# Performance work log

Measured on AMD Instinct MI355X. Metric: run time of the kernel, lower is better.

Reference implementation:

```python
import jax, jax.numpy as jnp
import numpy as np

N, D, E, K = 65536, 2048, 64, 8
EPS = 1e-5


def setup_inputs() -> dict:
    key = jax.random.key(0)
    kx, kw = jax.random.split(key)
    x = jax.random.normal(kx, (N, D), dtype=jnp.float32)
    # nn.Linear(input_size, num_experts, bias=False) weight: [E, D]
    W = jax.random.normal(kw, (E, D), dtype=jnp.float32) * (1.0 / np.sqrt(D))
    return {"x": x, "W": W}


def _l1_normalize(v):
    # torch F.normalize(p=1, dim=0): v / max(||v||_1, 1e-12)
    return v / jnp.maximum(jnp.sum(jnp.abs(v)), 1e-12)


def reference(x, W):
    # router logits: [N, E] in float32 (matches .float() in torch code)
    logits = (x @ W.T).astype(jnp.float32)
    top_v, top_i = jax.lax.top_k(logits, K)            # [N, K]
    top_k_gates = jax.nn.softmax(top_v, axis=-1).astype(x.dtype)
    # training-branch aux loss (compute_aux_loss)
    probs = jax.nn.softmax(logits, axis=-1)            # [N, E]
    rows = jnp.arange(logits.shape[0])[:, None]
    dense_gates = jnp.zeros_like(probs, dtype=top_k_gates.dtype).at[rows, top_i].set(top_k_gates)
    probs_sum = probs.sum(0)                           # [E]
    freq = (dense_gates > 0).astype(jnp.float32).sum(0)  # [E]
    # log(sum(exp(logits)) + eps)^2 summed, computed stably
    lse = jnp.logaddexp(jax.scipy.special.logsumexp(logits, axis=-1), jnp.log(EPS))
    zloss = jnp.sum(lse ** 2) / logits.shape[0]
    switchloss = E * jnp.sum(_l1_normalize(probs_sum) * _l1_normalize(freq))
    loss = switchloss + 0.1 * zloss
    return top_i, top_k_gates, loss
```

## Files before the change

### kernel.cpp

```cpp
#include <hip/hip_runtime.h>
#include <math.h>

#define NROWS 65536
#define DDIM 2048
#define NEXP 64
#define TOPK 8

constexpr int BM = 128;
constexpr int BK = 32;
constexpr int NTH = 256;
constexpr int NSTEP = DDIM / BK;
constexpr int CAP = 8192;
constexpr float THR = 3e-4f;

typedef short bf16x8 __attribute__((ext_vector_type(8)));
typedef float f32x4 __attribute__((ext_vector_type(4)));

__device__ inline unsigned short bfround(float f) {
    union { float f; unsigned u; } v; v.f = f;
    unsigned r = (v.u + 0x7fffu + ((v.u >> 16) & 1u)) >> 16;
    return (unsigned short)r;
}
__device__ inline float bf2f(unsigned short h) {
    union { unsigned u; float f; } v; v.u = ((unsigned)h) << 16;
    return v.f;
}
__device__ inline void cvt8(const float4& A, const float4& B, bf16x8& h, bf16x8& l) {
    float f[8] = {A.x, A.y, A.z, A.w, B.x, B.y, B.z, B.w};
#pragma unroll
    for (int j = 0; j < 8; ++j) {
        unsigned short hh = bfround(f[j]);
        h[j] = (short)hh;
        l[j] = (short)bfround(f[j] - bf2f(hh));
    }
}

__global__ __launch_bounds__(NTH, 1)
void gate_kernel(const float* __restrict__ x, const float* __restrict__ W,
                 float* __restrict__ out_idx, float* __restrict__ out_gate,
                 float* __restrict__ g_psum, float* __restrict__ g_freq,
                 float* __restrict__ g_zsum, int* __restrict__ g_cnt,
                 int* __restrict__ g_rows, float* __restrict__ g_logits)
{
    __shared__ __align__(16) short Bfrag[2][2][4][64][8];
    __shared__ float psum_s[NEXP];
    __shared__ float fcnt_s[NEXP];

    const int tid = threadIdx.x;
    const int w = tid >> 6;
    const int lane = tid & 63;
    const int g = lane >> 4;
    const int c = lane & 15;
    const int row0 = blockIdx.x * BM + w * 32;

    if (tid < NEXP) { psum_s[tid] = 0.f; fcnt_s[tid] = 0.f; }

    const int se = tid >> 2;
    const int skg = tid & 3;
    const int sct = se >> 4;
    const int slane = (se & 15) + (skg << 4);

    const float* xr0 = x + (size_t)(row0 + c) * DDIM + g * 8;
    const float* xr1 = x + (size_t)(row0 + 16 + c) * DDIM + g * 8;
    const float* wp  = W + (size_t)se * DDIM + skg * 8;

    f32x4 acc[2][4];
#pragma unroll
    for (int rt = 0; rt < 2; ++rt)
#pragma unroll
        for (int ct = 0; ct < 4; ++ct) acc[rt][ct] = (f32x4){0.f, 0.f, 0.f, 0.f};

    float4 xa[2][2], xb[2][2];

    auto stageB = [&](int k0, int buf) {
        float4 a = *reinterpret_cast<const float4*>(wp + k0);
        float4 b = *reinterpret_cast<const float4*>(wp + k0 + 4);
        bf16x8 h, l;
        cvt8(a, b, h, l);
        *reinterpret_cast<bf16x8*>(&Bfrag[buf][0][sct][slane][0]) = h;
        *reinterpret_cast<bf16x8*>(&Bfrag[buf][1][sct][slane][0]) = l;
    };

    xa[0][0] = *reinterpret_cast<const float4*>(xr0);
    xa[0][1] = *reinterpret_cast<const float4*>(xr0 + 4);
    xa[1][0] = *reinterpret_cast<const float4*>(xr1);
    xa[1][1] = *reinterpret_cast<const float4*>(xr1 + 4);
    stageB(0, 0);
    __syncthreads();

    for (int t = 0; t < NSTEP; ++t) {
        const int buf = t & 1;
        const int kn = (t + 1) * BK;
        if (t + 1 < NSTEP) {
            xb[0][0] = *reinterpret_cast<const float4*>(xr0 + kn);
            xb[0][1] = *reinterpret_cast<const float4*>(xr0 + kn + 4);
            xb[1][0] = *reinterpret_cast<const float4*>(xr1 + kn);
            xb[1][1] = *reinterpret_cast<const float4*>(xr1 + kn + 4);
            stageB(kn, buf ^ 1);
        }
        bf16x8 ah[2], al[2];
        cvt8(xa[0][0], xa[0][1], ah[0], al[0]);
        cvt8(xa[1][0], xa[1][1], ah[1], al[1]);
        bf16x8 bh[4], bl[4];
#pragma unroll
        for (int ct = 0; ct < 4; ++ct) {
            bh[ct] = *reinterpret_cast<const bf16x8*>(&Bfrag[buf][0][ct][lane][0]);
            bl[ct] = *reinterpret_cast<const bf16x8*>(&Bfrag[buf][1][ct][lane][0]);
        }
#pragma unroll
        for (int rt = 0; rt < 2; ++rt)
#pragma unroll
            for (int ct = 0; ct < 4; ++ct) {
                acc[rt][ct] = __builtin_amdgcn_mfma_f32_16x16x32_bf16(
                    ah[rt], bh[ct], acc[rt][ct], 0, 0, 0);
                acc[rt][ct] = __builtin_amdgcn_mfma_f32_16x16x32_bf16(
                    ah[rt], bl[ct], acc[rt][ct], 0, 0, 0);
                acc[rt][ct] = __builtin_amdgcn_mfma_f32_16x16x32_bf16(
                    al[rt], bh[ct], acc[rt][ct], 0, 0, 0);
            }
#pragma unroll
        for (int rt = 0; rt < 2; ++rt)
#pragma unroll
            for (int i = 0; i < 2; ++i) xa[rt][i] = xb[rt][i];
        __syncthreads();
    }

    float pcol[4] = {0.f, 0.f, 0.f, 0.f};
    float zsq_acc = 0.f;

#pragma unroll
    for (int rt = 0; rt < 2; ++rt) {
#pragma unroll
        for (int reg = 0; reg < 4; ++reg) {
            const int row = row0 + rt * 16 + g * 4 + reg;
            float ld[4];
#pragma unroll
            for (int ct = 0; ct < 4; ++ct) ld[ct] = acc[rt][ct][reg];

            float tv[9]; int ti[9];
#pragma unroll
            for (int p = 0; p < 9; ++p) {
                float bv = -3.4e38f; int bgi = 127;
#pragma unroll
                for (int ct = 0; ct < 4; ++ct) {
                    int e = ct * 16 + c;
                    if (ld[ct] > bv) { bv = ld[ct]; bgi = e; }
                }
#pragma unroll
                for (int m = 1; m < 16; m <<= 1) {
                    float ov = __shfl_xor(bv, m, 16);
                    int ogi = __shfl_xor(bgi, m, 16);
                    if (ov > bv || (ov == bv && ogi < bgi)) { bv = ov; bgi = ogi; }
                }
                tv[p] = bv; ti[p] = bgi;
#pragma unroll
                for (int ct = 0; ct < 4; ++ct)
                    if (bgi == ct * 16 + c) ld[ct] = -3.4e38f;
            }

            float mg = 3.4e38f;
#pragma unroll
            for (int p = 0; p < 8; ++p) mg = fminf(mg, tv[p] - tv[p + 1]);
            if (mg < THR) {
                int idx = 0;
                if (c == 0) idx = atomicAdd(g_cnt, 1);
                idx = __shfl(idx, (lane >> 4) << 4, 64);
                if (idx < CAP) {
                    if (c == 0) g_rows[idx] = row;
#pragma unroll
                    for (int ct = 0; ct < 4; ++ct)
                        g_logits[(size_t)idx * NEXP + ct * 16 + c] = acc[rt][ct][reg];
                }
            }

            const float m0 = tv[0];
            float pe[4], ps = 0.f;
#pragma unroll
            for (int ct = 0; ct < 4; ++ct) {
                pe[ct] = expf(acc[rt][ct][reg] - m0);
                ps += pe[ct];
            }
            float s = ps;
#pragma unroll
            for (int m = 1; m < 16; m <<= 1) s += __shfl_xor(s, m, 16);
            const float inv_s = 1.f / s;
#pragma unroll
            for (int ct = 0; ct < 4; ++ct) pcol[ct] += pe[ct] * inv_s;

            if (c == 0) {
                float lsef = m0 + logf(s);
                const float lb = -11.512925464970229f;
                float mx = fmaxf(lsef, lb), mn = fminf(lsef, lb);
                float z = mx + log1pf(expf(mn - mx));
                zsq_acc += z * z;
            }

            float gs = 0.f;
#pragma unroll
            for (int p = 0; p < 8; ++p) gs += expf(tv[p] - m0);
            if (c < 8) {
                float mytv = tv[0]; int myti = ti[0];
#pragma unroll
                for (int p = 1; p < 8; ++p)
                    if (c == p) { mytv = tv[p]; myti = ti[p]; }
                const size_t base = (size_t)row * TOPK;
                out_idx[base + c] = (float)myti;
                out_gate[base + c] = expf(mytv - m0) / gs;
                atomicAdd(&fcnt_s[myti], 1.f);
            }
        }
    }

#pragma unroll
    for (int off = 32; off > 0; off >>= 1) zsq_acc += __shfl_down(zsq_acc, off, 64);
    if (lane == 0) atomicAdd(g_zsum, zsq_acc);

#pragma unroll
    for (int ct = 0; ct < 4; ++ct) atomicAdd(&psum_s[ct * 16 + c], pcol[ct]);
    __syncthreads();
    if (tid < NEXP) {
        atomicAdd(&g_psum[tid], psum_s[tid]);
        atomicAdd(&g_freq[tid], fcnt_s[tid]);
    }
}

__global__ __launch_bounds__(256, 1)
void fixup_kernel(const float* __restrict__ x, const float* __restrict__ W,
                  float* __restrict__ out_idx, float* __restrict__ out_gate,
                  const int* __restrict__ g_cnt, const int* __restrict__ g_rows,
                  const float* __restrict__ g_logits)
{
    const int n = min(*g_cnt, CAP);
    const int tid = threadIdx.x;
    const int grp = tid >> 5;
    const int gl = tid & 31;
    __shared__ float sLog[NEXP];
    __shared__ double sD[16];
    __shared__ int sCand[16];
    __shared__ int sNc;

    for (int i = blockIdx.x; i < n; i += gridDim.x) {
        const int row = g_rows[i];
        if (tid < NEXP) sLog[tid] = g_logits[(size_t)i * NEXP + tid];
        if (tid == 0) sNc = 0;
        __syncthreads();

        if (tid < NEXP) {
            const int lane = tid;
            const float myv = sLog[lane];
            float vv = myv;
            float v9 = 0.f;
#pragma unroll
            for (int p = 0; p < 9; ++p) {
                float bv = vv; int bgi = lane;
#pragma unroll
                for (int m = 1; m < 64; m <<= 1) {
                    float ov = __shfl_xor(bv, m, 64);
                    int ogi = __shfl_xor(bgi, m, 64);
                    if (ov > bv || (ov == bv && ogi < bgi)) { bv = ov; bgi = ogi; }
                }
                if (lane == bgi) vv = -3.4e38f;
                v9 = bv;
            }
            if (myv >= v9 - THR) {
                int slot = atomicAdd(&sNc, 1);
                if (slot < 16) sCand[slot] = lane;
            }
        }
        __syncthreads();
        const int nc = min(sNc, 16);

        const float* xr = x + (size_t)row * DDIM;
        for (int cb = 0; cb < nc; cb += 8) {
            const int ci = cb + grp;
            if (ci < nc) {
                const float* wr = W + (size_t)sCand[ci] * DDIM;
                double p0 = 0.0, p1 = 0.0, p2 = 0.0, p3 = 0.0;
#pragma unroll
                for (int j = 0; j < 16; ++j) {
                    const int k = j * 128 + gl * 4;
                    float4 wv = *reinterpret_cast<const float4*>(wr + k);
                    float4 xv = *reinterpret_cast<const float4*>(xr + k);
                    p0 = fma((double)xv.x, (double)wv.x, p0);
                    p1 = fma((double)xv.y, (double)wv.y, p1);
                    p2 = fma((double)xv.z, (double)wv.z, p2);
                    p3 = fma((double)xv.w, (double)wv.w, p3);
                }
                double s = (p0 + p1) + (p2 + p3);
#pragma unroll
                for (int m = 1; m < 32; m <<= 1) s += __shfl_xor(s, m, 32);
                if (gl == 0) sD[ci] = s;
            }
        }
        __syncthreads();

        if (tid < NEXP) {
            const int lane = tid;
            double v = (lane < nc) ? sD[lane] : -HUGE_VAL;
            int id = (lane < nc) ? sCand[lane] : 1000;
            double tv[8]; int ti[8];
#pragma unroll
            for (int p = 0; p < 8; ++p) {
                double bv = v; int bgi = id;
#pragma unroll
                for (int m = 1; m < 64; m <<= 1) {
                    double ov = __shfl_xor(bv, m, 64);
                    int ogi = __shfl_xor(bgi, m, 64);
                    if (ov > bv || (ov == bv && ogi < bgi)) { bv = ov; bgi = ogi; }
                }
                tv[p] = bv; ti[p] = bgi;
                if (id == bgi) v = -HUGE_VAL;
            }

            const double m0 = tv[0];
            double gs = 0.0, ge[8];
#pragma unroll
            for (int j = 0; j < 8; ++j) { ge[j] = exp(tv[j] - m0); gs += ge[j]; }
            if (lane < 8) {
                double myge = ge[0]; int myti = ti[0];
#pragma unroll
                for (int j = 1; j < 8; ++j)
                    if (lane == j) { myge = ge[j]; myti = ti[j]; }
                const size_t base = (size_t)row * TOPK;
                out_idx[base + lane] = (float)myti;
                out_gate[base + lane] = (float)(myge / gs);
            }
        }
        __syncthreads();
    }
}

__global__ void finalize_kernel(const float* __restrict__ g_psum,
                                const float* __restrict__ g_freq,
                                const float* __restrict__ g_zsum,
                                float* __restrict__ out_loss)
{
    const int lane = threadIdx.x & 63;
    float p = g_psum[lane], f = g_freq[lane];
    float sp = p, sf = f;
#pragma unroll
    for (int m = 1; m < 64; m <<= 1) { sp += __shfl_xor(sp, m, 64); sf += __shfl_xor(sf, m, 64); }
    sp = fmaxf(sp, 1e-12f);
    sf = fmaxf(sf, 1e-12f);
    float term = (p / sp) * (f / sf);
#pragma unroll
    for (int m = 1; m < 64; m <<= 1) term += __shfl_xor(term, m, 64);
    if (lane == 0)
        out_loss[0] = (float)NEXP * term + 0.1f * (g_zsum[0] / (float)NROWS);
}

extern "C" void kernel_launch(void* const* d_in, const int* in_sizes, int n_in,
                              void* d_out, int out_size, void* d_ws, size_t ws_size,
                              hipStream_t stream)
{
    const float* x = (const float*)d_in[0];
    const float* W = (const float*)d_in[1];
    float* out = (float*)d_out;
    float* out_idx  = out;
    float* out_gate = out + (size_t)NROWS * TOPK;
    float* out_loss = out + (size_t)2 * NROWS * TOPK;

    float* acc    = (float*)d_ws;
    int*   cnt    = (int*)d_ws + 129;
    int*   rows   = (int*)d_ws + 130;
    float* logits = (float*)d_ws + 130 + CAP;
    hipMemsetAsync(d_ws, 0, 130 * sizeof(float), stream);

    gate_kernel<<<NROWS / BM, NTH, 0, stream>>>(
        x, W, out_idx, out_gate, acc, acc + NEXP, acc + 2 * NEXP, cnt, rows, logits);
    fixup_kernel<<<2048, 256, 0, stream>>>(x, W, out_idx, out_gate, cnt, rows, logits);
    finalize_kernel<<<1, 64, 0, stream>>>(acc, acc + NEXP, acc + 2 * NEXP, out_loss);
}
```

Measured before the change: 237.5 us.

## Precompute bf16 split W fragments and fix ambiguous rows in-block

A new prep kernel converts W once into hi/lo bf16 MFMA fragments in workspace. The main GEMM loop then reads them straight from global/L2 instead of converting and staging W through shared memory every step, which also removes the per-step barrier. Rows with near-tied top-k logits are now recomputed in fp64 inside the gate kernel using per-wave shared buffers, with only overflow rows going to a smaller fixup launch. The trade-offs are an extra kernel launch, more global fragment loads per wave, and serial fp64 work in the gate kernel's tail.

```diff
diff --git a/kernel.cpp b/kernel.cpp
--- a/kernel.cpp
+++ b/kernel.cpp
@@ -7,11 +7,12 @@
 #define TOPK 8
 
 constexpr int BM = 128;
-constexpr int BK = 32;
 constexpr int NTH = 256;
-constexpr int NSTEP = DDIM / BK;
-constexpr int CAP = 8192;
+constexpr int NSTEP = 64;
+constexpr int CAP = 1024;
+constexpr int FCAP = 16;
 constexpr float THR = 3e-4f;
+constexpr int WFRAG_STEP = 4096;
 
 typedef short bf16x8 __attribute__((ext_vector_type(8)));
 typedef float f32x4 __attribute__((ext_vector_type(4)));
@@ -35,16 +36,37 @@
     }
 }
 
+__global__ __launch_bounds__(256)
+void prep_kernel(const float* __restrict__ W, short* __restrict__ wfrag)
+{
+    const int t = blockIdx.x;
+    const int tid = threadIdx.x;
+    const int ct = tid >> 6, lane = tid & 63;
+    const int e = ct * 16 + (lane & 15);
+    const int k = t * 32 + (lane >> 4) * 8;
+    const float* wp = W + (size_t)e * DDIM + k;
+    float4 a = *reinterpret_cast<const float4*>(wp);
+    float4 b = *reinterpret_cast<const float4*>(wp + 4);
+    bf16x8 h, l;
+    cvt8(a, b, h, l);
+    short* base = wfrag + (size_t)t * WFRAG_STEP;
+    *reinterpret_cast<bf16x8*>(base + (ct * 64 + lane) * 8) = h;
+    *reinterpret_cast<bf16x8*>(base + 2048 + (ct * 64 + lane) * 8) = l;
+}
+
 __global__ __launch_bounds__(NTH, 1)
-void gate_kernel(const float* __restrict__ x, const float* __restrict__ W,
+void gate_kernel(const float* __restrict__ x, const short* __restrict__ wfrag,
+                 const float* __restrict__ W,
                  float* __restrict__ out_idx, float* __restrict__ out_gate,
                  float* __restrict__ g_psum, float* __restrict__ g_freq,
                  float* __restrict__ g_zsum, int* __restrict__ g_cnt,
                  int* __restrict__ g_rows, float* __restrict__ g_logits)
 {
-    __shared__ __align__(16) short Bfrag[2][2][4][64][8];
     __shared__ float psum_s[NEXP];
     __shared__ float fcnt_s[NEXP];
+    __shared__ float fRow[4][FCAP][NEXP];
+    __shared__ int fId[4][FCAP];
+    __shared__ int fN[4];
 
     const int tid = threadIdx.x;
     const int w = tid >> 6;
@@ -54,15 +76,11 @@
     const int row0 = blockIdx.x * BM + w * 32;
 
     if (tid < NEXP) { psum_s[tid] = 0.f; fcnt_s[tid] = 0.f; }
-
-    const int se = tid >> 2;
-    const int skg = tid & 3;
-    const int sct = se >> 4;
-    const int slane = (se & 15) + (skg << 4);
+    if (lane == 0) fN[w] = 0;
+    __syncthreads();
 
     const float* xr0 = x + (size_t)(row0 + c) * DDIM + g * 8;
     const float* xr1 = x + (size_t)(row0 + 16 + c) * DDIM + g * 8;
-    const float* wp  = W + (size_t)se * DDIM + skg * 8;
 
     f32x4 acc[2][4];
 #pragma unroll
@@ -71,42 +89,29 @@
         for (int ct = 0; ct < 4; ++ct) acc[rt][ct] = (f32x4){0.f, 0.f, 0.f, 0.f};
 
     float4 xa[2][2], xb[2][2];
-
-    auto stageB = [&](int k0, int buf) {
-        float4 a = *reinterpret_cast<const float4*>(wp + k0);
-        float4 b = *reinterpret_cast<const float4*>(wp + k0 + 4);
-        bf16x8 h, l;
-        cvt8(a, b, h, l);
-        *reinterpret_cast<bf16x8*>(&Bfrag[buf][0][sct][slane][0]) = h;
-        *reinterpret_cast<bf16x8*>(&Bfrag[buf][1][sct][slane][0]) = l;
-    };
-
     xa[0][0] = *reinterpret_cast<const float4*>(xr0);
     xa[0][1] = *reinterpret_cast<const float4*>(xr0 + 4);
     xa[1][0] = *reinterpret_cast<const float4*>(xr1);
     xa[1][1] = *reinterpret_cast<const float4*>(xr1 + 4);
-    stageB(0, 0);
-    __syncthreads();
 
     for (int t = 0; t < NSTEP; ++t) {
-        const int buf = t & 1;
-        const int kn = (t + 1) * BK;
+        const short* wt = wfrag + (size_t)t * WFRAG_STEP;
+        bf16x8 bh[4], bl[4];
+#pragma unroll
+        for (int ct = 0; ct < 4; ++ct) {
+            bh[ct] = *reinterpret_cast<const bf16x8*>(wt + (ct * 64 + lane) * 8);
+            bl[ct] = *reinterpret_cast<const bf16x8*>(wt + 2048 + (ct * 64 + lane) * 8);
+        }
+        const int kn = (t + 1) * 32;
         if (t + 1 < NSTEP) {
             xb[0][0] = *reinterpret_cast<const float4*>(xr0 + kn);
             xb[0][1] = *reinterpret_cast<const float4*>(xr0 + kn + 4);
             xb[1][0] = *reinterpret_cast<const float4*>(xr1 + kn);
             xb[1][1] = *reinterpret_cast<const float4*>(xr1 + kn + 4);
-            stageB(kn, buf ^ 1);
         }
         bf16x8 ah[2], al[2];
         cvt8(xa[0][0], xa[0][1], ah[0], al[0]);
         cvt8(xa[1][0], xa[1][1], ah[1], al[1]);
-        bf16x8 bh[4], bl[4];
-#pragma unroll
-        for (int ct = 0; ct < 4; ++ct) {
-            bh[ct] = *reinterpret_cast<const bf16x8*>(&Bfrag[buf][0][ct][lane][0]);
-            bl[ct] = *reinterpret_cast<const bf16x8*>(&Bfrag[buf][1][ct][lane][0]);
-        }
 #pragma unroll
         for (int rt = 0; rt < 2; ++rt)
 #pragma unroll
@@ -122,7 +127,6 @@
         for (int rt = 0; rt < 2; ++rt)
 #pragma unroll
             for (int i = 0; i < 2; ++i) xa[rt][i] = xb[rt][i];
-        __syncthreads();
     }
 
     float pcol[4] = {0.f, 0.f, 0.f, 0.f};
@@ -161,15 +165,26 @@
             float mg = 3.4e38f;
 #pragma unroll
             for (int p = 0; p < 8; ++p) mg = fminf(mg, tv[p] - tv[p + 1]);
-            if (mg < THR) {
-                int idx = 0;
-                if (c == 0) idx = atomicAdd(g_cnt, 1);
-                idx = __shfl(idx, (lane >> 4) << 4, 64);
-                if (idx < CAP) {
-                    if (c == 0) g_rows[idx] = row;
+            const bool flagged = (mg < THR);
+            if (flagged) {
+                int slot = 0;
+                if (c == 0) slot = atomicAdd(&fN[w], 1);
+                slot = __shfl(slot, (lane >> 4) << 4, 64);
+                if (slot < FCAP) {
+                    if (c == 0) fId[w][slot] = row;
 #pragma unroll
                     for (int ct = 0; ct < 4; ++ct)
-                        g_logits[(size_t)idx * NEXP + ct * 16 + c] = acc[rt][ct][reg];
+                        fRow[w][slot][ct * 16 + c] = acc[rt][ct][reg];
+                } else {
+                    int idx = 0;
+                    if (c == 0) idx = atomicAdd(g_cnt, 1);
+                    idx = __shfl(idx, (lane >> 4) << 4, 64);
+                    if (idx < CAP) {
+                        if (c == 0) g_rows[idx] = row;
+#pragma unroll
+                        for (int ct = 0; ct < 4; ++ct)
+                            g_logits[(size_t)idx * NEXP + ct * 16 + c] = acc[rt][ct][reg];
+                    }
                 }
             }
 
@@ -206,8 +221,85 @@
                 const size_t base = (size_t)row * TOPK;
                 out_idx[base + c] = (float)myti;
                 out_gate[base + c] = expf(mytv - m0) / gs;
-                atomicAdd(&fcnt_s[myti], 1.f);
-            }
+                if (!flagged) atomicAdd(&fcnt_s[myti], 1.f);
+            }
+        }
+    }
+
+    const int nf = min(fN[w], FCAP);
+    for (int s = 0; s < nf; ++s) {
+        const int R = fId[w][s];
+        const float myLog = fRow[w][s][lane];
+        float vv = myLog, v9 = 0.f;
+#pragma unroll
+        for (int p = 0; p < 9; ++p) {
+            float bv = vv; int bgi = lane;
+#pragma unroll
+            for (int m = 1; m < 64; m <<= 1) {
+                float ov = __shfl_xor(bv, m, 64);
+                int ogi = __shfl_xor(bgi, m, 64);
+                if (ov > bv || (ov == bv && ogi < bgi)) { bv = ov; bgi = ogi; }
+            }
+            v9 = bv;
+            if (lane == bgi) vv = -3.4e38f;
+        }
+        const bool cand = (myLog >= v9 - THR);
+        unsigned long long cm = __ballot(cand);
+
+        const float* xrw = x + (size_t)R * DDIM;
+        float4 xv[8];
+#pragma unroll
+        for (int j = 0; j < 8; ++j)
+            xv[j] = *reinterpret_cast<const float4*>(xrw + j * 256 + lane * 4);
+
+        double myD = -HUGE_VAL;
+        unsigned long long m2 = cm;
+        while (m2) {
+            const int e = (int)__ffsll((unsigned long long)m2) - 1;
+            m2 &= (m2 - 1);
+            const float* wrp = W + (size_t)e * DDIM;
+            double p0 = 0.0, p1 = 0.0, p2 = 0.0, p3 = 0.0;
+#pragma unroll
+            for (int j = 0; j < 8; ++j) {
+                float4 wv = *reinterpret_cast<const float4*>(wrp + j * 256 + lane * 4);
+                p0 = fma((double)xv[j].x, (double)wv.x, p0);
+                p1 = fma((double)xv[j].y, (double)wv.y, p1);
+                p2 = fma((double)xv[j].z, (double)wv.z, p2);
+                p3 = fma((double)xv[j].w, (double)wv.w, p3);
+            }
+            double sd = (p0 + p1) + (p2 + p3);
+#pragma unroll
+            for (int m = 1; m < 64; m <<= 1) sd += __shfl_xor(sd, m, 64);
+            if (lane == e) myD = sd;
+        }
+
+        double v = cand ? myD : -HUGE_VAL;
+        double tvd[8]; int tid8[8];
+#pragma unroll
+        for (int p = 0; p < 8; ++p) {
+            double bv = v; int bgi = lane;
+#pragma unroll
+            for (int m = 1; m < 64; m <<= 1) {
+                double ov = __shfl_xor(bv, m, 64);
+                int ogi = __shfl_xor(bgi, m, 64);
+                if (ov > bv || (ov == bv && ogi < bgi)) { bv = ov; bgi = ogi; }
+            }
+            tvd[p] = bv; tid8[p] = bgi;
+            if (lane == bgi) v = -HUGE_VAL;
+        }
+        const double m0 = tvd[0];
+        double gsum = 0.0, ge[8];
+#pragma unroll
+        for (int j = 0; j < 8; ++j) { ge[j] = exp(tvd[j] - m0); gsum += ge[j]; }
+        if (lane < 8) {
+            double myge = ge[0]; int myti = tid8[0];
+#pragma unroll
+            for (int j = 1; j < 8; ++j)
+                if (lane == j) { myge = ge[j]; myti = tid8[j]; }
+            const size_t base = (size_t)R * TOPK;
+            out_idx[base + lane] = (float)myti;
+            out_gate[base + lane] = (float)(myge / gsum);
+            atomicAdd(&fcnt_s[myti], 1.f);
         }
     }
 
@@ -227,6 +319,7 @@
 __global__ __launch_bounds__(256, 1)
 void fixup_kernel(const float* __restrict__ x, const float* __restrict__ W,
                   float* __restrict__ out_idx, float* __restrict__ out_gate,
+                  float* __restrict__ g_freq,
                   const int* __restrict__ g_cnt, const int* __restrict__ g_rows,
                   const float* __restrict__ g_logits)
 {
@@ -248,8 +341,7 @@
         if (tid < NEXP) {
             const int lane = tid;
             const float myv = sLog[lane];
-            float vv = myv;
-            float v9 = 0.f;
+            float vv = myv, v9 = 0.f;
 #pragma unroll
             for (int p = 0; p < 9; ++p) {
                 float bv = vv; int bgi = lane;
@@ -280,16 +372,16 @@
                 for (int j = 0; j < 16; ++j) {
                     const int k = j * 128 + gl * 4;
                     float4 wv = *reinterpret_cast<const float4*>(wr + k);
-                    float4 xv = *reinterpret_cast<const float4*>(xr + k);
-                    p0 = fma((double)xv.x, (double)wv.x, p0);
-                    p1 = fma((double)xv.y, (double)wv.y, p1);
-                    p2 = fma((double)xv.z, (double)wv.z, p2);
-                    p3 = fma((double)xv.w, (double)wv.w, p3);
-                }
-                double s = (p0 + p1) + (p2 + p3);
-#pragma unroll
-                for (int m = 1; m < 32; m <<= 1) s += __shfl_xor(s, m, 32);
-                if (gl == 0) sD[ci] = s;
+                    float4 xvv = *reinterpret_cast<const float4*>(xr + k);
+                    p0 = fma((double)xvv.x, (double)wv.x, p0);
+                    p1 = fma((double)xvv.y, (double)wv.y, p1);
+                    p2 = fma((double)xvv.z, (double)wv.z, p2);
+                    p3 = fma((double)xvv.w, (double)wv.w, p3);
+                }
+                double sd = (p0 + p1) + (p2 + p3);
+#pragma unroll
+                for (int m = 1; m < 32; m <<= 1) sd += __shfl_xor(sd, m, 32);
+                if (gl == 0) sD[ci] = sd;
             }
         }
         __syncthreads();
@@ -311,7 +403,6 @@
                 tv[p] = bv; ti[p] = bgi;
                 if (id == bgi) v = -HUGE_VAL;
             }
-
             const double m0 = tv[0];
             double gs = 0.0, ge[8];
 #pragma unroll
@@ -324,6 +415,7 @@
                 const size_t base = (size_t)row * TOPK;
                 out_idx[base + lane] = (float)myti;
                 out_gate[base + lane] = (float)(myge / gs);
+                atomicAdd(&g_freq[myti], 1.0f);
             }
         }
         __syncthreads();
@@ -364,10 +456,14 @@
     int*   cnt    = (int*)d_ws + 129;
     int*   rows   = (int*)d_ws + 130;
     float* logits = (float*)d_ws + 130 + CAP;
+    short* wfrag  = (short*)((float*)d_ws + 66704);
     hipMemsetAsync(d_ws, 0, 130 * sizeof(float), stream);
 
+    prep_kernel<<<NSTEP, 256, 0, stream>>>(W, wfrag);
     gate_kernel<<<NROWS / BM, NTH, 0, stream>>>(
-        x, W, out_idx, out_gate, acc, acc + NEXP, acc + 2 * NEXP, cnt, rows, logits);
-    fixup_kernel<<<2048, 256, 0, stream>>>(x, W, out_idx, out_gate, cnt, rows, logits);
+        x, wfrag, W, out_idx, out_gate, acc, acc + NEXP, acc + 2 * NEXP,
+        cnt, rows, logits);
+    fixup_kernel<<<64, 256, 0, stream>>>(x, W, out_idx, out_gate, acc + NEXP,
+                                         cnt, rows, logits);
     finalize_kernel<<<1, 64, 0, stream>>>(acc, acc + NEXP, acc + 2 * NEXP, out_loss);
 }
```

New measurement: 268.6 us. +13.1%, slower.
